# Kernel tuning notes

Hardware: AMD Instinct MI355X
Metric: run time of the kernel (lower is better)

The kernel has to match this reference:

```python
import jax, jax.numpy as jnp
import numpy as np

EPS = 1e-8  # torch F.cosine_similarity eps


def setup_inputs() -> dict:
    key = jax.random.key(0)
    B, CAP, CD, CTX = 32, 32768, 64, 64
    ks = jax.random.split(key, 9)
    inp = {
        "query_content": jax.random.normal(ks[0], (B, CD), jnp.float32),
        "query_context": jax.random.normal(ks[1], (B, CTX), jnp.float32),
        "memory_content": 0.1 * jax.random.normal(ks[2], (CAP, CD), jnp.float32),
        "memory_contexts": 0.1 * jax.random.normal(ks[3], (CAP, CTX), jnp.float32),
        "memory_freshness": jnp.ones((CAP,), jnp.float32),
        "W1": jax.random.normal(ks[4], (2 * CD, CD), jnp.float32) / np.sqrt(2 * CD),
        "b1": 0.01 * jax.random.normal(ks[5], (CD,), jnp.float32),
        "W2": jax.random.normal(ks[6], (CD, 1), jnp.float32) / np.sqrt(CD),
        "b2": 0.01 * jax.random.normal(ks[7], (1,), jnp.float32),
        "top_k": 16,
    }
    return inp


def reference(query_content, query_context, memory_content, memory_contexts,
              memory_freshness, W1, b1, W2, b2, top_k):
    B, CD = query_content.shape
    # similarity_calculator MLP over all (query, memory) pairs.
    # Linear on concat([q, m]) == q @ W1[:CD] + m @ W1[CD:]  (avoids the concat).
    q_part = query_content @ W1[:CD]            # [B, CD]
    m_part = memory_content @ W1[CD:]           # [CAP, CD]
    h = jax.nn.relu(q_part[:, None, :] + m_part[None, :, :] + b1)  # [B, CAP, CD]
    content_sim = jax.nn.sigmoid(jnp.einsum('bch,h->bc', h, W2[:, 0]) + b2[0])  # [B, CAP]

    # cosine similarity between query_context and each stored context
    qn = query_context / jnp.maximum(jnp.linalg.norm(query_context, axis=-1, keepdims=True), EPS)
    mn = memory_contexts / jnp.maximum(jnp.linalg.norm(memory_contexts, axis=-1, keepdims=True), EPS)
    context_sim = qn @ mn.T                      # [B, CAP]

    time_weights = memory_freshness              # time_mask is all-ones in source
    final = 0.5 * content_sim + 0.3 * context_sim + 0.2 * time_weights[None, :]

    top_similarities, top_indices = jax.lax.top_k(final, top_k)   # [B, k]
    retrieved_content = memory_content[top_indices]               # [B, k, CD]
    retrieved_time_weights = time_weights[top_indices]            # [B, k]
    return (retrieved_content, top_similarities, retrieved_time_weights)
```

## Files before the change

### kernel.cpp

```cpp
#include <hip/hip_runtime.h>
#include <math.h>

#define CAP   32768
#define NB    32
#define ROWS  64
#define NBLK  (CAP / ROWS)
#define TOPK  16
#define CEPS  1e-8f

#define PITCH 68
#define CHUNK 1024
#define NCHUNK (CAP / CHUNK)

#define WS_QP    0
#define WS_QN    2048
#define WS_FINAL 4096

__global__ __launch_bounds__(64) void prep_kernel(
    const float* __restrict__ qc,
    const float* __restrict__ qctx,
    const float* __restrict__ W1,
    const float* __restrict__ b1,
    float* __restrict__ ws)
{
    const int b = blockIdx.x;
    const int j = threadIdx.x;

    float a0 = b1[j], a1 = 0.f, a2 = 0.f, a3 = 0.f;
    #pragma unroll
    for (int i = 0; i < 64; i += 4) {
        a0 = fmaf(qc[b * 64 + i + 0], W1[(i + 0) * 64 + j], a0);
        a1 = fmaf(qc[b * 64 + i + 1], W1[(i + 1) * 64 + j], a1);
        a2 = fmaf(qc[b * 64 + i + 2], W1[(i + 2) * 64 + j], a2);
        a3 = fmaf(qc[b * 64 + i + 3], W1[(i + 3) * 64 + j], a3);
    }
    ws[WS_QP + b * 64 + j] = (a0 + a1) + (a2 + a3);

    float x = qctx[b * 64 + j];
    float ss = x * x;
    ss += __shfl_xor(ss, 1,  64);
    ss += __shfl_xor(ss, 2,  64);
    ss += __shfl_xor(ss, 4,  64);
    ss += __shfl_xor(ss, 8,  64);
    ss += __shfl_xor(ss, 16, 64);
    ss += __shfl_xor(ss, 32, 64);
    ws[WS_QN + b * 64 + j] = x / fmaxf(sqrtf(ss), CEPS);
}

__global__ __launch_bounds__(256) void score_kernel(
    const float* __restrict__ mcont,
    const float* __restrict__ mctx,
    const float* __restrict__ fresh,
    const float* __restrict__ W1,
    const float* __restrict__ W2,
    const float* __restrict__ b2,
    float* __restrict__ ws)
{
    __shared__ float s_mc[ROWS * PITCH];
    __shared__ float s_qp[NB * PITCH];
    __shared__ float s_qn[NB * PITCH];
    __shared__ float s_base[ROWS];
    __shared__ float s_inv[ROWS];

    const int tid = threadIdx.x;
    const int C0 = blockIdx.x * ROWS;

    const float4* g_mc = (const float4*)(mcont + (size_t)C0 * 64);
    #pragma unroll
    for (int t = tid; t < ROWS * 16; t += 256) {
        int r = t >> 4, c4 = t & 15;
        *(float4*)&s_mc[r * PITCH + c4 * 4] = g_mc[t];
    }
    const float4* g_qp = (const float4*)(ws + WS_QP);
    const float4* g_qn = (const float4*)(ws + WS_QN);
    #pragma unroll
    for (int t = tid; t < NB * 16; t += 256) {
        int r = t >> 4, c4 = t & 15;
        *(float4*)&s_qp[r * PITCH + c4 * 4] = g_qp[t];
        *(float4*)&s_qn[r * PITCH + c4 * 4] = g_qn[t];
    }
    {
        const int r = tid >> 2, q = tid & 3;
        const float* xr = mctx + (size_t)(C0 + r) * 64 + q * 16;
        float ss = 0.f;
        #pragma unroll
        for (int i = 0; i < 4; ++i) {
            float4 x = *(const float4*)&xr[i * 4];
            ss = fmaf(x.x, x.x, ss); ss = fmaf(x.y, x.y, ss);
            ss = fmaf(x.z, x.z, ss); ss = fmaf(x.w, x.w, ss);
        }
        ss += __shfl_xor(ss, 1, 64);
        ss += __shfl_xor(ss, 2, 64);
        if (q == 0) {
            s_inv[r]  = 0.3f / fmaxf(sqrtf(ss), CEPS);
            s_base[r] = 0.2f * fresh[C0 + r];
        }
    }
    __syncthreads();

    const int c_lo = tid & 15;
    const int j0 = (tid >> 4) * 4;
    {
        float acc[4][4] = {{0.f}};
        #pragma unroll 4
        for (int i4 = 0; i4 < 16; ++i4) {
            float4 w0 = *(const float4*)&W1[(64 + i4 * 4 + 0) * 64 + j0];
            float4 w1r = *(const float4*)&W1[(64 + i4 * 4 + 1) * 64 + j0];
            float4 w2r = *(const float4*)&W1[(64 + i4 * 4 + 2) * 64 + j0];
            float4 w3r = *(const float4*)&W1[(64 + i4 * 4 + 3) * 64 + j0];
            #pragma unroll
            for (int ci = 0; ci < 4; ++ci) {
                float4 m = *(const float4*)&s_mc[(c_lo + 16 * ci) * PITCH + i4 * 4];
                acc[ci][0] = fmaf(m.x, w0.x, acc[ci][0]);
                acc[ci][1] = fmaf(m.x, w0.y, acc[ci][1]);
                acc[ci][2] = fmaf(m.x, w0.z, acc[ci][2]);
                acc[ci][3] = fmaf(m.x, w0.w, acc[ci][3]);
                acc[ci][0] = fmaf(m.y, w1r.x, acc[ci][0]);
                acc[ci][1] = fmaf(m.y, w1r.y, acc[ci][1]);
                acc[ci][2] = fmaf(m.y, w1r.z, acc[ci][2]);
                acc[ci][3] = fmaf(m.y, w1r.w, acc[ci][3]);
                acc[ci][0] = fmaf(m.z, w2r.x, acc[ci][0]);
                acc[ci][1] = fmaf(m.z, w2r.y, acc[ci][1]);
                acc[ci][2] = fmaf(m.z, w2r.z, acc[ci][2]);
                acc[ci][3] = fmaf(m.z, w2r.w, acc[ci][3]);
                acc[ci][0] = fmaf(m.w, w3r.x, acc[ci][0]);
                acc[ci][1] = fmaf(m.w, w3r.y, acc[ci][1]);
                acc[ci][2] = fmaf(m.w, w3r.z, acc[ci][2]);
                acc[ci][3] = fmaf(m.w, w3r.w, acc[ci][3]);
            }
        }
        __syncthreads();
        #pragma unroll
        for (int jj = 0; jj < 4; ++jj)
            #pragma unroll
            for (int ci = 0; ci < 4; ++ci)
                s_mc[(j0 + jj) * PITCH + c_lo + 16 * ci] = acc[ci][jj];
    }
    __syncthreads();

    const int bq = (tid & 15) << 1;
    const int cq = (tid >> 4) << 2;
    float4 a1v[2];
    a1v[0] = make_float4(0.f, 0.f, 0.f, 0.f);
    a1v[1] = make_float4(0.f, 0.f, 0.f, 0.f);
    float a2[2][4] = {{0.f}};
    const float* mxb = mctx + (size_t)C0 * 64;

    #pragma unroll 4
    for (int j4 = 0; j4 < 16; ++j4) {
        const int jo = j4 * 4;
        float4 w2v = *(const float4*)(W2 + jo);
        float4 qp0 = *(const float4*)&s_qp[ bq      * PITCH + jo];
        float4 qp1 = *(const float4*)&s_qp[(bq + 1) * PITCH + jo];
        float4 qn0 = *(const float4*)&s_qn[ bq      * PITCH + jo];
        float4 qn1 = *(const float4*)&s_qn[(bq + 1) * PITCH + jo];
        float4 m0 = *(const float4*)&s_mc[(jo + 0) * PITCH + cq];
        float4 m1 = *(const float4*)&s_mc[(jo + 1) * PITCH + cq];
        float4 m2 = *(const float4*)&s_mc[(jo + 2) * PITCH + cq];
        float4 m3 = *(const float4*)&s_mc[(jo + 3) * PITCH + cq];

        #pragma unroll
        for (int bi = 0; bi < 2; ++bi) {
            float4 qp = bi ? qp1 : qp0;
            float4& av = a1v[bi];
            av.x = fmaf(fmaxf(qp.x + m0.x, 0.f), w2v.x, av.x);
            av.y = fmaf(fmaxf(qp.x + m0.y, 0.f), w2v.x, av.y);
            av.z = fmaf(fmaxf(qp.x + m0.z, 0.f), w2v.x, av.z);
            av.w = fmaf(fmaxf(qp.x + m0.w, 0.f), w2v.x, av.w);
            av.x = fmaf(fmaxf(qp.y + m1.x, 0.f), w2v.y, av.x);
            av.y = fmaf(fmaxf(qp.y + m1.y, 0.f), w2v.y, av.y);
            av.z = fmaf(fmaxf(qp.y + m1.z, 0.f), w2v.y, av.z);
            av.w = fmaf(fmaxf(qp.y + m1.w, 0.f), w2v.y, av.w);
            av.x = fmaf(fmaxf(qp.z + m2.x, 0.f), w2v.z, av.x);
            av.y = fmaf(fmaxf(qp.z + m2.y, 0.f), w2v.z, av.y);
            av.z = fmaf(fmaxf(qp.z + m2.z, 0.f), w2v.z, av.z);
            av.w = fmaf(fmaxf(qp.z + m2.w, 0.f), w2v.z, av.w);
            av.x = fmaf(fmaxf(qp.w + m3.x, 0.f), w2v.w, av.x);
            av.y = fmaf(fmaxf(qp.w + m3.y, 0.f), w2v.w, av.y);
            av.z = fmaf(fmaxf(qp.w + m3.z, 0.f), w2v.w, av.z);
            av.w = fmaf(fmaxf(qp.w + m3.w, 0.f), w2v.w, av.w);
        }
        #pragma unroll
        for (int ci = 0; ci < 4; ++ci) {
            float4 xv = *(const float4*)&mxb[(cq + ci) * 64 + jo];
            a2[0][ci] = fmaf(qn0.x, xv.x, a2[0][ci]);
            a2[0][ci] = fmaf(qn0.y, xv.y, a2[0][ci]);
            a2[0][ci] = fmaf(qn0.z, xv.z, a2[0][ci]);
            a2[0][ci] = fmaf(qn0.w, xv.w, a2[0][ci]);
            a2[1][ci] = fmaf(qn1.x, xv.x, a2[1][ci]);
            a2[1][ci] = fmaf(qn1.y, xv.y, a2[1][ci]);
            a2[1][ci] = fmaf(qn1.z, xv.z, a2[1][ci]);
            a2[1][ci] = fmaf(qn1.w, xv.w, a2[1][ci]);
        }
    }

    const float b2v = b2[0];
    float4 inv4  = *(const float4*)&s_inv[cq];
    float4 base4 = *(const float4*)&s_base[cq];
    #pragma unroll
    for (int bi = 0; bi < 2; ++bi) {
        float4 r;
        r.x = 0.5f / (1.f + expf(-(a1v[bi].x + b2v))) + a2[bi][0] * inv4.x + base4.x;
        r.y = 0.5f / (1.f + expf(-(a1v[bi].y + b2v))) + a2[bi][1] * inv4.y + base4.y;
        r.z = 0.5f / (1.f + expf(-(a1v[bi].z + b2v))) + a2[bi][2] * inv4.z + base4.z;
        r.w = 0.5f / (1.f + expf(-(a1v[bi].w + b2v))) + a2[bi][3] * inv4.w + base4.w;
        *(float4*)&ws[WS_FINAL + (size_t)(bq + bi) * CAP + C0 + cq] = r;
    }
}

__device__ __forceinline__ void bitonic64_desc(float& v, int& iv, int lane)
{
    #pragma unroll
    for (int k = 2; k <= 64; k <<= 1) {
        #pragma unroll
        for (int j = k >> 1; j > 0; j >>= 1) {
            float ov = __shfl_xor(v, j, 64);
            int   oi = __shfl_xor(iv, j, 64);
            bool low        = (lane & j) == 0;
            bool dirDesc    = (lane & k) == 0;
            bool takeBetter = (low == dirDesc);
            bool otherBetter = (ov > v) || (ov == v && oi < iv);
            if (otherBetter == takeBetter) { v = ov; iv = oi; }
        }
    }
}

__global__ __launch_bounds__(256) void topk_stage1(float* __restrict__ ws)
{
    __shared__ float s_val[64];
    __shared__ int   s_idx[64];

    const int lane = threadIdx.x & 63;
    const int w    = threadIdx.x >> 6;
    const int b    = blockIdx.y;
    float* row = ws + WS_FINAL + (size_t)b * CAP;
    const int cbase = blockIdx.x * CHUNK;
    const int sb = cbase + w * 256;

    float4 t = *(const float4*)&row[sb + lane * 4];
    float v0 = t.x, v1 = t.y, v2 = t.z, v3 = t.w;
    int   i0 = sb + lane * 4 + 0;
    int   i1 = sb + lane * 4 + 1;
    int   i2 = sb + lane * 4 + 2;
    int   i3 = sb + lane * 4 + 3;

    bitonic64_desc(v0, i0, lane);
    bitonic64_desc(v1, i1, lane);
    bitonic64_desc(v2, i2, lane);
    bitonic64_desc(v3, i3, lane);

    const int r = lane & 15;
    float c0 = __shfl(v0, r, 64), c1 = __shfl(v1, r, 64);
    float c2 = __shfl(v2, r, 64), c3 = __shfl(v3, r, 64);
    int   d0 = __shfl(i0, r, 64), d1 = __shfl(i1, r, 64);
    int   d2 = __shfl(i2, r, 64), d3 = __shfl(i3, r, 64);
    const int s = lane >> 4;
    float cv = (s == 0) ? c0 : (s == 1) ? c1 : (s == 2) ? c2 : c3;
    int   ci = (s == 0) ? d0 : (s == 1) ? d1 : (s == 2) ? d2 : d3;

    bitonic64_desc(cv, ci, lane);

    if (lane < TOPK) {
        s_val[w * TOPK + lane] = cv;
        s_idx[w * TOPK + lane] = ci;
    }
    __syncthreads();
    if (w != 0) return;

    float mv = s_val[lane];
    int   mi = s_idx[lane];
    bitonic64_desc(mv, mi, lane);
    if (lane < TOPK) {
        row[cbase + lane]        = mv;
        row[cbase + TOPK + lane] = __int_as_float(mi);
    }
}

__global__ __launch_bounds__(512) void topk_stage2(
    const float* __restrict__ mcont,
    const float* __restrict__ fresh,
    const float* __restrict__ ws,
    float* __restrict__ out)
{
    __shared__ float s_v1[128];
    __shared__ int   s_i1[128];
    __shared__ float s_v2[32];
    __shared__ int   s_i2[32];

    const int lane = threadIdx.x & 63;
    const int w    = threadIdx.x >> 6;
    const int b    = blockIdx.x;
    const float* row = ws + WS_FINAL + (size_t)b * CAP;

    {
        const int cand = w * 64 + lane;
        const int ch = cand >> 4, pos = cand & 15;
        float v  = row[ch * CHUNK + pos];
        int   iv = __float_as_int(row[ch * CHUNK + TOPK + pos]);
        bitonic64_desc(v, iv, lane);
        if (lane < TOPK) {
            s_v1[w * TOPK + lane] = v;
            s_i1[w * TOPK + lane] = iv;
        }
    }
    __syncthreads();

    if (w < 2) {
        float v  = s_v1[w * 64 + lane];
        int   iv = s_i1[w * 64 + lane];
        bitonic64_desc(v, iv, lane);
        if (lane < TOPK) {
            s_v2[w * TOPK + lane] = v;
            s_i2[w * TOPK + lane] = iv;
        }
    }
    __syncthreads();
    if (w != 0) return;

    float fv = (lane < 32) ? s_v2[lane] : -INFINITY;
    int   fi = (lane < 32) ? s_i2[lane] : 0x7FFFFFFF;
    bitonic64_desc(fv, fi, lane);

    float* out_content = out;
    float* out_sim     = out + NB * TOPK * 64;
    float* out_tw      = out + NB * TOPK * 64 + NB * TOPK;

    if (lane < TOPK) {
        out_sim[b * TOPK + lane] = fv;
        out_tw [b * TOPK + lane] = fresh[fi];
    }

    #pragma unroll
    for (int r = 0; r < TOPK; ++r) {
        int wi = __shfl(fi, r, 64);
        out_content[(size_t)b * TOPK * 64 + r * 64 + lane] =
            mcont[(size_t)wi * 64 + lane];
    }
}

extern "C" void kernel_launch(void* const* d_in, const int* in_sizes, int n_in,
                              void* d_out, int out_size, void* d_ws, size_t ws_size,
                              hipStream_t stream) {
    const float* qc    = (const float*)d_in[0];
    const float* qctx  = (const float*)d_in[1];
    const float* mcont = (const float*)d_in[2];
    const float* mctx  = (const float*)d_in[3];
    const float* fresh = (const float*)d_in[4];
    const float* W1    = (const float*)d_in[5];
    const float* b1    = (const float*)d_in[6];
    const float* W2    = (const float*)d_in[7];
    const float* b2    = (const float*)d_in[8];
    float* out = (float*)d_out;
    float* ws  = (float*)d_ws;

    prep_kernel<<<NB, 64, 0, stream>>>(qc, qctx, W1, b1, ws);
    score_kernel<<<NBLK, 256, 0, stream>>>(mcont, mctx, fresh, W1, W2, b2, ws);
    topk_stage1<<<dim3(NCHUNK, NB), 256, 0, stream>>>(ws);
    topk_stage2<<<NB, 512, 0, stream>>>(mcont, fresh, ws, out);
}
```

Before: 125.9 us.

## Fuse top-k stages via last-block-done atomic counter

Merges the two top-k kernels into one launch. Each chunk block writes its local top-16 to a dedicated workspace area and increments a per-query atomic counter. The last block to finish for a query does the final merge and the gather. This removes one kernel launch and the gap between launches, at the cost of threadfences, an atomic per block and a serialized tail in the last block. The counter is reset in prep_kernel.

```diff
diff --git a/kernel.cpp b/kernel.cpp
--- a/kernel.cpp
+++ b/kernel.cpp
@@ -15,6 +15,9 @@
 #define WS_QP    0
 #define WS_QN    2048
 #define WS_FINAL 4096
+#define WS_CVAL  (WS_FINAL + NB * CAP)
+#define WS_CIDX  (WS_CVAL + NB * NCHUNK * TOPK)
+#define WS_CNT   (WS_CIDX + NB * NCHUNK * TOPK)
 
 __global__ __launch_bounds__(64) void prep_kernel(
     const float* __restrict__ qc,
@@ -25,6 +28,8 @@
 {
     const int b = blockIdx.x;
     const int j = threadIdx.x;
+
+    if (j == 0) ((int*)ws)[WS_CNT + b] = 0;
 
     float a0 = b1[j], a1 = 0.f, a2 = 0.f, a3 = 0.f;
     #pragma unroll
@@ -225,10 +230,19 @@
     }
 }
 
-__global__ __launch_bounds__(256) void topk_stage1(float* __restrict__ ws)
+__global__ __launch_bounds__(256) void topk_fused(
+    const float* __restrict__ mcont,
+    const float* __restrict__ fresh,
+    float* __restrict__ ws,
+    float* __restrict__ out)
 {
     __shared__ float s_val[64];
     __shared__ int   s_idx[64];
+    __shared__ float s_v1[128];
+    __shared__ int   s_i1[128];
+    __shared__ float s_v2[32];
+    __shared__ int   s_i2[32];
+    __shared__ int   s_last;
 
     const int lane = threadIdx.x & 63;
     const int w    = threadIdx.x >> 6;
@@ -236,6 +250,10 @@
     float* row = ws + WS_FINAL + (size_t)b * CAP;
     const int cbase = blockIdx.x * CHUNK;
     const int sb = cbase + w * 256;
+
+    float* cval = ws + WS_CVAL + (size_t)b * (NCHUNK * TOPK);
+    int*   cidx = (int*)ws + WS_CIDX + (size_t)b * (NCHUNK * TOPK);
+    int*   cnt  = (int*)ws + WS_CNT;
 
     float4 t = *(const float4*)&row[sb + lane * 4];
     float v0 = t.x, v1 = t.y, v2 = t.z, v3 = t.w;
@@ -265,42 +283,37 @@
         s_idx[w * TOPK + lane] = ci;
     }
     __syncthreads();
-    if (w != 0) return;
-
-    float mv = s_val[lane];
-    int   mi = s_idx[lane];
-    bitonic64_desc(mv, mi, lane);
-    if (lane < TOPK) {
-        row[cbase + lane]        = mv;
-        row[cbase + TOPK + lane] = __int_as_float(mi);
-    }
-}
-
-__global__ __launch_bounds__(512) void topk_stage2(
-    const float* __restrict__ mcont,
-    const float* __restrict__ fresh,
-    const float* __restrict__ ws,
-    float* __restrict__ out)
-{
-    __shared__ float s_v1[128];
-    __shared__ int   s_i1[128];
-    __shared__ float s_v2[32];
-    __shared__ int   s_i2[32];
-
-    const int lane = threadIdx.x & 63;
-    const int w    = threadIdx.x >> 6;
-    const int b    = blockIdx.x;
-    const float* row = ws + WS_FINAL + (size_t)b * CAP;
-
-    {
-        const int cand = w * 64 + lane;
-        const int ch = cand >> 4, pos = cand & 15;
-        float v  = row[ch * CHUNK + pos];
-        int   iv = __float_as_int(row[ch * CHUNK + TOPK + pos]);
+
+    if (w == 0) {
+        float mv = s_val[lane];
+        int   mi = s_idx[lane];
+        bitonic64_desc(mv, mi, lane);
+        if (lane < TOPK) {
+            cval[blockIdx.x * TOPK + lane] = mv;
+            cidx[blockIdx.x * TOPK + lane] = mi;
+        }
+        __threadfence();
+        if (lane == 0) {
+            int old = atomicAdd(&cnt[b], 1);
+            s_last = (old == NCHUNK - 1) ? 1 : 0;
+        }
+    }
+    __syncthreads();
+    if (!s_last) return;
+
+    __threadfence();
+    volatile const float* vv = cval;
+    volatile const int*   vi = cidx;
+
+    #pragma unroll
+    for (int g = 0; g < 2; ++g) {
+        const int s2 = w + 4 * g;
+        float v  = vv[s2 * 64 + lane];
+        int   iv = vi[s2 * 64 + lane];
         bitonic64_desc(v, iv, lane);
         if (lane < TOPK) {
-            s_v1[w * TOPK + lane] = v;
-            s_i1[w * TOPK + lane] = iv;
+            s_v1[s2 * TOPK + lane] = v;
+            s_i1[s2 * TOPK + lane] = iv;
         }
     }
     __syncthreads();
@@ -331,9 +344,9 @@
     }
 
     #pragma unroll
-    for (int r = 0; r < TOPK; ++r) {
-        int wi = __shfl(fi, r, 64);
-        out_content[(size_t)b * TOPK * 64 + r * 64 + lane] =
+    for (int rr = 0; rr < TOPK; ++rr) {
+        int wi = __shfl(fi, rr, 64);
+        out_content[(size_t)b * TOPK * 64 + rr * 64 + lane] =
             mcont[(size_t)wi * 64 + lane];
     }
 }
@@ -355,6 +368,5 @@
 
     prep_kernel<<<NB, 64, 0, stream>>>(qc, qctx, W1, b1, ws);
     score_kernel<<<NBLK, 256, 0, stream>>>(mcont, mctx, fresh, W1, W2, b2, ws);
-    topk_stage1<<<dim3(NCHUNK, NB), 256, 0, stream>>>(ws);
-    topk_stage2<<<NB, 512, 0, stream>>>(mcont, fresh, ws, out);
-}
+    topk_fused<<<dim3(NCHUNK, NB), 256, 0, stream>>>(mcont, fresh, ws, out);
+}
```

After: 153.4 us. 1.22x slower.
